# Performance work log

Hardware: AMD Instinct MI355X
Metric: run time of the kernel (lower is better)

## Reference

```python
import jax, jax.numpy as jnp
import numpy as np

B, C, H, W = 8, 256, 64, 64
CI = 128  # inter_channels = in_channels // reduction

def _conv1x1(x, w, b):
    # x: [b, c, h, w], w: [o, c], b: [o]
    return jnp.einsum('bchw,oc->bohw', x, w) + b[None, :, None, None]

def setup_inputs() -> dict:
    key = jax.random.key(0)
    ks = jax.random.split(key, 5)
    s_in = 1.0 / np.sqrt(C)
    s_ci = 1.0 / np.sqrt(CI)
    return {
        'x': jax.random.normal(ks[0], (B, C, H, W), jnp.float32),
        'w_g': jax.random.normal(ks[1], (CI, C), jnp.float32) * s_in,
        'b_g': jnp.zeros((CI,), jnp.float32),
        'w_theta': jax.random.normal(ks[2], (CI, C), jnp.float32) * s_in,
        'b_theta': jnp.zeros((CI,), jnp.float32),
        'w_phi': jax.random.normal(ks[3], (CI, C), jnp.float32) * s_in,
        'b_phi': jnp.zeros((CI,), jnp.float32),
        'w_out': jax.random.normal(ks[4], (C, CI), jnp.float32) * s_ci,
        'b_out': jnp.zeros((C,), jnp.float32),
    }

def reference(x, w_g, b_g, w_theta, b_theta, w_phi, b_phi, w_out, b_out):
    n, c, h, w = x.shape
    N = h * w
    g_x = _conv1x1(x, w_g, b_g).reshape(n, CI, N).transpose(0, 2, 1)        # [b, N, ci]
    theta_x = _conv1x1(x, w_theta, b_theta).reshape(n, CI, N).transpose(0, 2, 1)  # [b, N, ci]
    phi_x = _conv1x1(x, w_phi, b_phi).reshape(n, CI, N)                     # [b, ci, N]
    pw = jnp.einsum('bnc,bcm->bnm', theta_x, phi_x)                         # [b, N, N]
    # Faithful to source: divides by ci**(-0.5) == multiplies by sqrt(ci)
    pw = pw / (jnp.asarray(CI, x.dtype) ** -0.5)
    pw = jax.nn.softmax(pw, axis=-1)
    y = jnp.einsum('bnm,bmc->bnc', pw, g_x)                                 # [b, N, ci]
    y = y.transpose(0, 2, 1).reshape(n, CI, h, w)
    return x + _conv1x1(y, w_out, b_out)
```

## Files before the change

### kernel.cpp

```cpp
#include <hip/hip_runtime.h>
#include <hip/hip_bf16.h>
#include <stdint.h>
#include <stddef.h>


typedef __bf16 bf16;
typedef __attribute__((ext_vector_type(8))) __bf16 bf16x8;
typedef __attribute__((ext_vector_type(4))) __bf16 bf16x4;
typedef __attribute__((ext_vector_type(4))) float  f32x4;
typedef __attribute__((ext_vector_type(4))) int    i32x4;

#define MFMA16(a, b, c) __builtin_amdgcn_mfma_f32_16x16x32_bf16((a), (b), (c), 0, 0, 0)

constexpr int NB  = 8;
constexpr int NC  = 256;
constexpr int NN  = 4096;
constexpr int NCI = 128;
constexpr size_t NEL = (size_t)NB * NN * NCI;
constexpr int PBATCH = NN * NCI;

#define QSCALE (11.313708498984761f * 1.4426950408889634f)


__global__ __launch_bounds__(256) void k_proj(
    const float* __restrict__ x,
    const float* __restrict__ wt, const float* __restrict__ bt,
    const float* __restrict__ wp, const float* __restrict__ bp,
    const float* __restrict__ wg, const float* __restrict__ bg,
    bf16* __restrict__ qh, bf16* __restrict__ ql,
    bf16* __restrict__ kh, bf16* __restrict__ kl,
    bf16* __restrict__ vv)
{
    const int nt  = blockIdx.x;
    const int pj  = blockIdx.y;
    const int b   = blockIdx.z;
    const int tid = threadIdx.x;
    const int wv  = tid >> 6;
    const int ln  = tid & 63;
    const int lg  = ln >> 4;
    const int lq  = ln & 15;

    const float* W;
    const float* bias;
    if (pj == 0)      { W = wt; bias = bt; }
    else if (pj == 1) { W = wp; bias = bp; }
    else              { W = wg; bias = bg; }
    const bool split = (pj != 2);

    __shared__ char lds[49152];
    char* Ah = lds;
    char* Al = lds + 8192;
    char* Wh = lds + 16384;
    char* Wl = lds + 32768;

    f32x4 acc[8];
#pragma unroll
    for (int j = 0; j < 8; ++j) acc[j] = f32x4{0.f, 0.f, 0.f, 0.f};

    const int n0 = nt * 64;

    for (int c0 = 0; c0 < NC; c0 += 64) {
        __syncthreads();
#pragma unroll
        for (int p = 0; p < 4; ++p) {
            int cc = p * 16 + (tid >> 4);
            int nn = (tid & 15) * 4;
            f32x4 xv = *(const f32x4*)(x + ((size_t)b * NC + (c0 + cc)) * NN + n0 + nn);
#pragma unroll
            for (int e = 0; e < 4; ++e) {
                float f = xv[e];
                bf16 hh = (bf16)f;
                int row = nn + e;
                int off = (row * 128 + cc * 2) ^ ((row & 7) << 4);
                *(bf16*)(Ah + off) = hh;
                *(bf16*)(Al + off) = (bf16)(f - (float)hh);
            }
        }
#pragma unroll
        for (int p = 0; p < 8; ++p) {
            int i  = p * 16 + (tid >> 4);
            int c4 = (tid & 15) * 4;
            f32x4 w4 = *(const f32x4*)(W + (size_t)i * NC + c0 + c4);
            bf16x4 hv, lv;
#pragma unroll
            for (int e = 0; e < 4; ++e) {
                bf16 hh = (bf16)w4[e];
                hv[e] = hh;
                lv[e] = (bf16)(w4[e] - (float)hh);
            }
            int off = (i * 128 + c4 * 2) ^ ((i & 7) << 4);
            *(bf16x4*)(Wh + off) = hv;
            if (split) *(bf16x4*)(Wl + off) = lv;
        }
        __syncthreads();
#pragma unroll
        for (int kk = 0; kk < 2; ++kk) {
            int row  = wv * 16 + lq;
            int koff = kk * 64 + lg * 16;
            int aoff = (row * 128 + koff) ^ ((row & 7) << 4);
            bf16x8 ah = *(const bf16x8*)(Ah + aoff);
            bf16x8 al = *(const bf16x8*)(Al + aoff);
#pragma unroll
            for (int j = 0; j < 8; ++j) {
                int ir   = j * 16 + lq;
                int woff = (ir * 128 + koff) ^ ((ir & 7) << 4);
                bf16x8 bh = *(const bf16x8*)(Wh + woff);
                acc[j] = MFMA16(ah, bh, acc[j]);
                if (split) {
                    bf16x8 bl = *(const bf16x8*)(Wl + woff);
                    acc[j] = MFMA16(ah, bl, acc[j]);
                    acc[j] = MFMA16(al, bh, acc[j]);
                }
            }
        }
    }

    if (pj == 2) {
        __syncthreads();
        char* T = lds;
#pragma unroll
        for (int j = 0; j < 8; ++j) {
            int i = j * 16 + lq;
            float bv2 = bias[i];
#pragma unroll
            for (int r = 0; r < 4; ++r) {
                int nl = wv * 16 + lg * 4 + r;
                int off = (i * 128 + nl * 2) ^ ((i & 7) << 4);
                *(bf16*)(T + off) = (bf16)(acc[j][r] + bv2);
            }
        }
        __syncthreads();
#pragma unroll
        for (int p = 0; p < 4; ++p) {
            int i  = p * 32 + (tid >> 3);
            int sl = tid & 7;
            i32x4 tv = *(const i32x4*)(T + ((i * 128 + sl * 16) ^ ((i & 7) << 4)));
            size_t off = (size_t)b * PBATCH
                       + (size_t)((((nt * 8 + (i >> 4)) * 2 + (sl >> 2)) * 64
                                   + (sl & 3) * 16 + (i & 15)) * 8);
            *(i32x4*)(vv + off) = tv;
        }
    } else {
        const float sc = (pj == 0) ? QSCALE : 1.0f;
#pragma unroll
        for (int j = 0; j < 8; ++j) {
            int i = j * 16 + lq;
            float bv2 = bias[i];
#pragma unroll
            for (int r = 0; r < 4; ++r) {
                int q = n0 + wv * 16 + lg * 4 + r;
                size_t off = ((size_t)b * NN + q) * NCI + i;
                float val = (acc[j][r] + bv2) * sc;
                bf16 hh = (bf16)val;
                bf16 ll = (bf16)(val - (float)hh);
                if (pj == 0) { qh[off] = hh; ql[off] = ll; }
                else         { kh[off] = hh; kl[off] = ll; }
            }
        }
    }
}

__global__ __launch_bounds__(128, 2) void k_attn_sp(
    const bf16* __restrict__ qh, const bf16* __restrict__ ql,
    const bf16* __restrict__ kh, const bf16* __restrict__ kl,
    const bf16* __restrict__ vf,
    bf16* __restrict__ p0, bf16* __restrict__ p1, float* __restrict__ ml)
{
    const int bid = blockIdx.x;
    const int b   = bid & 7;
    const int rs  = bid >> 3;
    const int qt  = rs & 63;
    const int h   = rs >> 6;
    const int tid = threadIdx.x;
    const int wv  = tid >> 6;
    const int ln  = tid & 63;
    const int lg  = ln >> 4;
    const int lq  = ln & 15;
    const int n0  = qt * 64;
    const int mb0 = h * 2048;
    bf16* ph = h ? p1 : p0;

    __shared__ __attribute__((aligned(16))) char lds[36864];
    char* P = lds + 32768 + wv * 2048;

    const int smm = tid >> 4;
    const int ssl = tid & 15;

    bf16x8 qhf[2][4], qlf[2][4];
#pragma unroll
    for (int q2 = 0; q2 < 2; ++q2) {
        int qrow = n0 + wv * 32 + q2 * 16 + lq;
        const bf16* bh = qh + ((size_t)b * NN + qrow) * NCI;
        const bf16* bl = ql + ((size_t)b * NN + qrow) * NCI;
#pragma unroll
        for (int kk = 0; kk < 4; ++kk) {
            qhf[q2][kk] = *(const bf16x8*)(bh + kk * 32 + lg * 8);
            qlf[q2][kk] = *(const bf16x8*)(bl + kk * 32 + lg * 8);
        }
    }

    f32x4 o[2][8];
#pragma unroll
    for (int q2 = 0; q2 < 2; ++q2)
#pragma unroll
        for (int j = 0; j < 8; ++j) o[q2][j] = f32x4{0.f, 0.f, 0.f, 0.f};
    float mrun[2] = {-1e30f, -1e30f};
    float lrun[2] = {0.f, 0.f};

    const bf16* vb = vf + (size_t)b * PBATCH + (size_t)ln * 8;

    {
#pragma unroll
        for (int p = 0; p < 4; ++p) {
            int mm = p * 8 + smm;
            size_t g = ((size_t)b * NN + mb0 + mm) * NCI + ssl * 8;
            i32x4 hv = *(const i32x4*)(kh + g);
            i32x4 lv = *(const i32x4*)(kl + g);
            int off = (mm * 256 + ssl * 16) ^ ((mm & 7) << 4);
            *(i32x4*)(lds + off) = hv;
            *(i32x4*)(lds + 8192 + off) = lv;
        }
    }
    __syncthreads();

    for (int t = 0; t < 64; ++t) {
        const int cur = t & 1;
        char* KHc = lds + cur * 16384;
        char* KLc = KHc + 8192;
        char* KHn = lds + (cur ^ 1) * 16384;
        char* KLn = KHn + 8192;
        const bool pre = (t < 63);

        i32x4 rkh[4], rkl[4];
        if (pre) {
#pragma unroll
            for (int p = 0; p < 4; ++p) {
                size_t g = ((size_t)b * NN + mb0 + (t + 1) * 32 + p * 8 + smm) * NCI + ssl * 8;
                rkh[p] = *(const i32x4*)(kh + g);
                rkl[p] = *(const i32x4*)(kl + g);
            }
        }
        __builtin_amdgcn_sched_barrier(0);

        f32x4 s[2][2];
        __builtin_amdgcn_s_setprio(1);
#pragma unroll
        for (int jm = 0; jm < 2; ++jm) {
            s[jm][0] = f32x4{0.f, 0.f, 0.f, 0.f};
            s[jm][1] = f32x4{0.f, 0.f, 0.f, 0.f};
            const int mrow = jm * 16 + lq;
            const int sw = (mrow & 7) << 4;
#pragma unroll
            for (int kk = 0; kk < 4; ++kk) {
                int aoff = (mrow * 256 + kk * 64 + lg * 16) ^ sw;
                bf16x8 ah = *(const bf16x8*)(KHc + aoff);
                bf16x8 al = *(const bf16x8*)(KLc + aoff);
                s[jm][0] = MFMA16(ah, qhf[0][kk], s[jm][0]);
                s[jm][1] = MFMA16(ah, qhf[1][kk], s[jm][1]);
                s[jm][0] = MFMA16(al, qhf[0][kk], s[jm][0]);
                s[jm][1] = MFMA16(al, qhf[1][kk], s[jm][1]);
                s[jm][0] = MFMA16(ah, qlf[0][kk], s[jm][0]);
                s[jm][1] = MFMA16(ah, qlf[1][kk], s[jm][1]);
            }
        }
        __builtin_amdgcn_s_setprio(0);

        bf16x8 bv[8];
        {
            const bf16* vp = vb + (size_t)(h * 32 + (t >> 1)) * 8192;
#pragma unroll
            for (int j = 0; j < 8; ++j)
                bv[j] = *(const bf16x8*)(vp + (j * 2 + (t & 1)) * 512);
        }
        __builtin_amdgcn_sched_barrier(0);

        if (pre) {
#pragma unroll
            for (int p = 0; p < 4; ++p) {
                int mm = p * 8 + smm;
                int off = (mm * 256 + ssl * 16) ^ ((mm & 7) << 4);
                *(i32x4*)(KHn + off) = rkh[p];
                *(i32x4*)(KLn + off) = rkl[p];
            }
        }

        float tm[2];
        tm[0] = s[0][0][0];
        tm[1] = s[0][1][0];
#pragma unroll
        for (int jm = 0; jm < 2; ++jm)
#pragma unroll
            for (int r = 0; r < 4; ++r) {
                tm[0] = fmaxf(tm[0], s[jm][0][r]);
                tm[1] = fmaxf(tm[1], s[jm][1][r]);
            }
#pragma unroll
        for (int q2 = 0; q2 < 2; ++q2) {
            tm[q2] = fmaxf(tm[q2], __shfl_xor(tm[q2], 16));
            tm[q2] = fmaxf(tm[q2], __shfl_xor(tm[q2], 32));
        }

        bool grow = (tm[0] > mrun[0] + 8.f) || (tm[1] > mrun[1] + 8.f);
        if (__any(grow)) {
            float alpha[2];
#pragma unroll
            for (int q2 = 0; q2 < 2; ++q2) {
                float mnew = fmaxf(mrun[q2], tm[q2]);
                alpha[q2] = exp2f(mrun[q2] - mnew);
                mrun[q2] = mnew;
                lrun[q2] *= alpha[q2];
            }
            float av0[4], av1[4];
#pragma unroll
            for (int r = 0; r < 4; ++r) {
                av0[r] = __shfl(alpha[0], lg * 4 + r);
                av1[r] = __shfl(alpha[1], lg * 4 + r);
            }
#pragma unroll
            for (int j = 0; j < 8; ++j)
#pragma unroll
                for (int r = 0; r < 4; ++r) {
                    o[0][j][r] *= av0[r];
                    o[1][j][r] *= av1[r];
                }
        }

        float psum[2] = {0.f, 0.f};
#pragma unroll
        for (int jm = 0; jm < 2; ++jm)
#pragma unroll
            for (int q2 = 0; q2 < 2; ++q2) {
                bf16x4 pk;
#pragma unroll
                for (int r = 0; r < 4; ++r) {
                    float e2 = exp2f(s[jm][q2][r] - mrun[q2]);
                    psum[q2] += e2;
                    pk[r] = (bf16)e2;
                }
                int row = q2 * 16 + lq;
                int off = (row * 64 + (jm * 16 + lg * 4) * 2) ^ ((row & 7) << 4);
                *(bf16x4*)(P + off) = pk;
            }
#pragma unroll
        for (int q2 = 0; q2 < 2; ++q2) {
            psum[q2] += __shfl_xor(psum[q2], 16);
            psum[q2] += __shfl_xor(psum[q2], 32);
            lrun[q2] += psum[q2];
        }

        bf16x8 pa[2];
#pragma unroll
        for (int q2 = 0; q2 < 2; ++q2) {
            int row = q2 * 16 + lq;
            pa[q2] = *(const bf16x8*)(P + ((row * 64 + lg * 16) ^ ((row & 7) << 4)));
        }
        __builtin_amdgcn_s_setprio(1);
#pragma unroll
        for (int j = 0; j < 8; ++j) {
            o[0][j] = MFMA16(pa[0], bv[j], o[0][j]);
            o[1][j] = MFMA16(pa[1], bv[j], o[1][j]);
        }
        __builtin_amdgcn_s_setprio(0);

        __syncthreads();
    }

    float rl0[4], rl1[4];
#pragma unroll
    for (int r = 0; r < 4; ++r) {
        rl0[r] = 1.f / __shfl(lrun[0], lg * 4 + r);
        rl1[r] = 1.f / __shfl(lrun[1], lg * 4 + r);
    }
#pragma unroll
    for (int j = 0; j < 8; ++j) {
        int d = j * 16 + lq;
#pragma unroll
        for (int r = 0; r < 4; ++r) {
            int q0 = n0 + wv * 32 + lg * 4 + r;
            ph[((size_t)b * NN + q0) * NCI + d]      = (bf16)(o[0][j][r] * rl0[r]);
            ph[((size_t)b * NN + q0 + 16) * NCI + d] = (bf16)(o[1][j][r] * rl1[r]);
        }
    }
    if (lg == 0) {
#pragma unroll
        for (int q2 = 0; q2 < 2; ++q2) {
            int row = n0 + wv * 32 + q2 * 16 + lq;
            size_t base = ((size_t)b * NN + row) * 4 + h * 2;
            ml[base]     = mrun[q2];
            ml[base + 1] = lrun[q2];
        }
    }
}

__global__ __launch_bounds__(256) void k_comb(
    const bf16* __restrict__ p0, const bf16* __restrict__ p1,
    const float* __restrict__ ml, bf16* __restrict__ y)
{
    int row = blockIdx.x * 16 + (threadIdx.x >> 4);
    int d0  = (threadIdx.x & 15) * 8;
    f32x4 q = *(const f32x4*)(ml + (size_t)row * 4);
    float M  = fmaxf(q[0], q[2]);
    float w0 = exp2f(q[0] - M) * q[1];
    float w1 = exp2f(q[2] - M) * q[3];
    float inv = 1.f / (w0 + w1);
    w0 *= inv; w1 *= inv;
    size_t off = (size_t)row * NCI + d0;
    bf16x8 a = *(const bf16x8*)(p0 + off);
    bf16x8 c = *(const bf16x8*)(p1 + off);
    bf16x8 r;
#pragma unroll
    for (int e = 0; e < 8; ++e) r[e] = (bf16)(w0 * (float)a[e] + w1 * (float)c[e]);
    *(bf16x8*)(y + off) = r;
}

__global__ __launch_bounds__(256) void k_out(
    const bf16* __restrict__ y, const float* __restrict__ x,
    const float* __restrict__ w_out, const float* __restrict__ b_out,
    float* __restrict__ out)
{
    const int nt  = blockIdx.x;
    const int b   = blockIdx.y;
    const int tid = threadIdx.x;
    const int wv  = tid >> 6;
    const int ln  = tid & 63;
    const int lg  = ln >> 4;
    const int lq  = ln & 15;
    const int n0  = nt * 64;

    __shared__ char Y[16384];
#pragma unroll
    for (int p = 0; p < 4; ++p) {
        int nn = p * 16 + (tid >> 4);
        int d0 = (tid & 15) * 8;
        i32x4 t = *(const i32x4*)(y + ((size_t)b * NN + n0 + nn) * NCI + d0);
        *(i32x4*)(Y + ((nn * 256 + d0 * 2) ^ ((nn & 7) << 4))) = t;
    }
    __syncthreads();

    bf16x8 af[4];
    {
        int row = wv * 16 + lq;
#pragma unroll
        for (int kk = 0; kk < 4; ++kk) {
            int koff = kk * 64 + lg * 16;
            af[kk] = *(const bf16x8*)(Y + ((row * 256 + koff) ^ ((row & 7) << 4)));
        }
    }

    f32x4 acc[16];
#pragma unroll
    for (int j = 0; j < 16; ++j) acc[j] = f32x4{0.f, 0.f, 0.f, 0.f};

#pragma unroll
    for (int j = 0; j < 16; ++j) {
        int c = j * 16 + lq;
#pragma unroll
        for (int kk = 0; kk < 4; ++kk) {
            int i0 = kk * 32 + lg * 8;
            f32x4 wa = *(const f32x4*)(w_out + (size_t)c * NCI + i0);
            f32x4 wb = *(const f32x4*)(w_out + (size_t)c * NCI + i0 + 4);
            bf16x8 bw;
#pragma unroll
            for (int e = 0; e < 4; ++e) { bw[e] = (bf16)wa[e]; bw[e + 4] = (bf16)wb[e]; }
            acc[j] = MFMA16(af[kk], bw, acc[j]);
        }
    }

#pragma unroll
    for (int j = 0; j < 16; ++j) {
        int c = j * 16 + lq;
        int nb = n0 + wv * 16 + lg * 4;
        size_t off = ((size_t)b * NC + c) * (size_t)NN + nb;
        f32x4 xv = *(const f32x4*)(x + off);
        float bo = b_out[c];
        f32x4 r;
#pragma unroll
        for (int t = 0; t < 4; ++t) r[t] = acc[j][t] + xv[t] + bo;
        *(f32x4*)(out + off) = r;
    }
}

extern "C" void kernel_launch(void* const* d_in, const int* in_sizes, int n_in,
                              void* d_out, int out_size, void* d_ws, size_t ws_size,
                              hipStream_t stream)
{
    (void)in_sizes; (void)n_in; (void)out_size; (void)ws_size;
    const float* x  = (const float*)d_in[0];
    const float* wg = (const float*)d_in[1];
    const float* bg = (const float*)d_in[2];
    const float* wt = (const float*)d_in[3];
    const float* bt = (const float*)d_in[4];
    const float* wp = (const float*)d_in[5];
    const float* bp = (const float*)d_in[6];
    const float* wo = (const float*)d_in[7];
    const float* bo = (const float*)d_in[8];
    float* out = (float*)d_out;

    char* ws = (char*)d_ws;
    bf16* qh = (bf16*)(ws);
    bf16* ql = (bf16*)(ws + NEL * 2);
    bf16* kh = (bf16*)(ws + NEL * 4);
    bf16* kl = (bf16*)(ws + NEL * 6);
    bf16* vv = (bf16*)(ws + NEL * 8);
    bf16* y  = qh;
    bf16* p0 = (bf16*)(ws + NEL * 10);
    bf16* p1 = (bf16*)(ws + NEL * 12);
    float* ml = (float*)(ws + NEL * 14);

    k_proj<<<dim3(64, 3, 8), 256, 0, stream>>>(x, wt, bt, wp, bp, wg, bg,
                                               qh, ql, kh, kl, vv);
    k_attn_sp<<<dim3(1024), 128, 0, stream>>>(qh, ql, kh, kl, vv, p0, p1, ml);
    k_comb<<<dim3(2048), 256, 0, stream>>>(p0, p1, ml, y);
    k_out<<<dim3(64, 8), 256, 0, stream>>>(y, x, wo, bo, out);
}
```

Baseline: 249.5 us.

## Fuse three projections per block, fold split-combine into output conv, hoist V loads

```diff
diff --git a/kernel.cpp b/kernel.cpp
--- a/kernel.cpp
+++ b/kernel.cpp
@@ -22,7 +22,7 @@
 #define QSCALE (11.313708498984761f * 1.4426950408889634f)
 
 
-__global__ __launch_bounds__(256) void k_proj(
+__global__ __launch_bounds__(256) void k_proj3(
     const float* __restrict__ x,
     const float* __restrict__ wt, const float* __restrict__ bt,
     const float* __restrict__ wp, const float* __restrict__ bp,
@@ -32,30 +32,24 @@
     bf16* __restrict__ vv)
 {
     const int nt  = blockIdx.x;
-    const int pj  = blockIdx.y;
-    const int b   = blockIdx.z;
+    const int b   = blockIdx.y;
     const int tid = threadIdx.x;
     const int wv  = tid >> 6;
     const int ln  = tid & 63;
     const int lg  = ln >> 4;
     const int lq  = ln & 15;
 
-    const float* W;
-    const float* bias;
-    if (pj == 0)      { W = wt; bias = bt; }
-    else if (pj == 1) { W = wp; bias = bp; }
-    else              { W = wg; bias = bg; }
-    const bool split = (pj != 2);
-
     __shared__ char lds[49152];
     char* Ah = lds;
     char* Al = lds + 8192;
     char* Wh = lds + 16384;
     char* Wl = lds + 32768;
 
-    f32x4 acc[8];
-#pragma unroll
-    for (int j = 0; j < 8; ++j) acc[j] = f32x4{0.f, 0.f, 0.f, 0.f};
+    f32x4 acc[3][8];
+#pragma unroll
+    for (int pj = 0; pj < 3; ++pj)
+#pragma unroll
+        for (int j = 0; j < 8; ++j) acc[pj][j] = f32x4{0.f, 0.f, 0.f, 0.f};
 
     const int n0 = nt * 64;
 
@@ -76,87 +70,93 @@
                 *(bf16*)(Al + off) = (bf16)(f - (float)hh);
             }
         }
-#pragma unroll
-        for (int p = 0; p < 8; ++p) {
-            int i  = p * 16 + (tid >> 4);
-            int c4 = (tid & 15) * 4;
-            f32x4 w4 = *(const f32x4*)(W + (size_t)i * NC + c0 + c4);
-            bf16x4 hv, lv;
-#pragma unroll
-            for (int e = 0; e < 4; ++e) {
-                bf16 hh = (bf16)w4[e];
-                hv[e] = hh;
-                lv[e] = (bf16)(w4[e] - (float)hh);
-            }
-            int off = (i * 128 + c4 * 2) ^ ((i & 7) << 4);
-            *(bf16x4*)(Wh + off) = hv;
-            if (split) *(bf16x4*)(Wl + off) = lv;
-        }
-        __syncthreads();
-#pragma unroll
-        for (int kk = 0; kk < 2; ++kk) {
-            int row  = wv * 16 + lq;
-            int koff = kk * 64 + lg * 16;
-            int aoff = (row * 128 + koff) ^ ((row & 7) << 4);
-            bf16x8 ah = *(const bf16x8*)(Ah + aoff);
-            bf16x8 al = *(const bf16x8*)(Al + aoff);
-#pragma unroll
-            for (int j = 0; j < 8; ++j) {
-                int ir   = j * 16 + lq;
-                int woff = (ir * 128 + koff) ^ ((ir & 7) << 4);
-                bf16x8 bh = *(const bf16x8*)(Wh + woff);
-                acc[j] = MFMA16(ah, bh, acc[j]);
-                if (split) {
-                    bf16x8 bl = *(const bf16x8*)(Wl + woff);
-                    acc[j] = MFMA16(ah, bl, acc[j]);
-                    acc[j] = MFMA16(al, bh, acc[j]);
+
+#pragma unroll
+        for (int pj = 0; pj < 3; ++pj) {
+            const float* W = (pj == 0) ? wt : (pj == 1) ? wp : wg;
+            const bool split = (pj != 2);
+            if (pj != 0) __syncthreads();
+#pragma unroll
+            for (int p = 0; p < 8; ++p) {
+                int i  = p * 16 + (tid >> 4);
+                int c4 = (tid & 15) * 4;
+                f32x4 w4 = *(const f32x4*)(W + (size_t)i * NC + c0 + c4);
+                bf16x4 hv, lv;
+#pragma unroll
+                for (int e = 0; e < 4; ++e) {
+                    bf16 hh = (bf16)w4[e];
+                    hv[e] = hh;
+                    lv[e] = (bf16)(w4[e] - (float)hh);
                 }
-            }
-        }
-    }
-
-    if (pj == 2) {
-        __syncthreads();
-        char* T = lds;
-#pragma unroll
-        for (int j = 0; j < 8; ++j) {
-            int i = j * 16 + lq;
-            float bv2 = bias[i];
-#pragma unroll
-            for (int r = 0; r < 4; ++r) {
-                int nl = wv * 16 + lg * 4 + r;
-                int off = (i * 128 + nl * 2) ^ ((i & 7) << 4);
-                *(bf16*)(T + off) = (bf16)(acc[j][r] + bv2);
-            }
-        }
-        __syncthreads();
-#pragma unroll
-        for (int p = 0; p < 4; ++p) {
-            int i  = p * 32 + (tid >> 3);
-            int sl = tid & 7;
-            i32x4 tv = *(const i32x4*)(T + ((i * 128 + sl * 16) ^ ((i & 7) << 4)));
-            size_t off = (size_t)b * PBATCH
-                       + (size_t)((((nt * 8 + (i >> 4)) * 2 + (sl >> 2)) * 64
-                                   + (sl & 3) * 16 + (i & 15)) * 8);
-            *(i32x4*)(vv + off) = tv;
-        }
-    } else {
-        const float sc = (pj == 0) ? QSCALE : 1.0f;
-#pragma unroll
-        for (int j = 0; j < 8; ++j) {
-            int i = j * 16 + lq;
-            float bv2 = bias[i];
-#pragma unroll
-            for (int r = 0; r < 4; ++r) {
-                int q = n0 + wv * 16 + lg * 4 + r;
-                size_t off = ((size_t)b * NN + q) * NCI + i;
-                float val = (acc[j][r] + bv2) * sc;
-                bf16 hh = (bf16)val;
-                bf16 ll = (bf16)(val - (float)hh);
-                if (pj == 0) { qh[off] = hh; ql[off] = ll; }
-                else         { kh[off] = hh; kl[off] = ll; }
-            }
-        }
+                int off = (i * 128 + c4 * 2) ^ ((i & 7) << 4);
+                *(bf16x4*)(Wh + off) = hv;
+                if (split) *(bf16x4*)(Wl + off) = lv;
+            }
+            __syncthreads();
+#pragma unroll
+            for (int kk = 0; kk < 2; ++kk) {
+                int row  = wv * 16 + lq;
+                int koff = kk * 64 + lg * 16;
+                int aoff = (row * 128 + koff) ^ ((row & 7) << 4);
+                bf16x8 ah = *(const bf16x8*)(Ah + aoff);
+                bf16x8 al = *(const bf16x8*)(Al + aoff);
+#pragma unroll
+                for (int j = 0; j < 8; ++j) {
+                    int ir   = j * 16 + lq;
+                    int woff = (ir * 128 + koff) ^ ((ir & 7) << 4);
+                    bf16x8 bh = *(const bf16x8*)(Wh + woff);
+                    acc[pj][j] = MFMA16(ah, bh, acc[pj][j]);
+                    if (split) {
+                        bf16x8 bl = *(const bf16x8*)(Wl + woff);
+                        acc[pj][j] = MFMA16(ah, bl, acc[pj][j]);
+                        acc[pj][j] = MFMA16(al, bh, acc[pj][j]);
+                    }
+                }
+            }
+        }
+    }
+
+#pragma unroll
+    for (int j = 0; j < 8; ++j) {
+        int i = j * 16 + lq;
+        float bvt = bt[i];
+        float bvp = bp[i];
+#pragma unroll
+        for (int r = 0; r < 4; ++r) {
+            int q = n0 + wv * 16 + lg * 4 + r;
+            size_t off = ((size_t)b * NN + q) * NCI + i;
+            float vt2 = (acc[0][j][r] + bvt) * QSCALE;
+            bf16 th = (bf16)vt2;
+            qh[off] = th; ql[off] = (bf16)(vt2 - (float)th);
+            float vp2 = acc[1][j][r] + bvp;
+            bf16 phh = (bf16)vp2;
+            kh[off] = phh; kl[off] = (bf16)(vp2 - (float)phh);
+        }
+    }
+
+    __syncthreads();
+    char* T = lds;
+#pragma unroll
+    for (int j = 0; j < 8; ++j) {
+        int i = j * 16 + lq;
+        float bv2 = bg[i];
+#pragma unroll
+        for (int r = 0; r < 4; ++r) {
+            int nl = wv * 16 + lg * 4 + r;
+            int off = (i * 128 + nl * 2) ^ ((i & 7) << 4);
+            *(bf16*)(T + off) = (bf16)(acc[2][j][r] + bv2);
+        }
+    }
+    __syncthreads();
+#pragma unroll
+    for (int p = 0; p < 4; ++p) {
+        int i  = p * 32 + (tid >> 3);
+        int sl = tid & 7;
+        i32x4 tv = *(const i32x4*)(T + ((i * 128 + sl * 16) ^ ((i & 7) << 4)));
+        size_t off = (size_t)b * PBATCH
+                   + (size_t)((((nt * 8 + (i >> 4)) * 2 + (sl >> 2)) * 64
+                               + (sl & 3) * 16 + (i & 15)) * 8);
+        *(i32x4*)(vv + off) = tv;
     }
 }
 
@@ -240,6 +240,13 @@
                 rkl[p] = *(const i32x4*)(kl + g);
             }
         }
+        bf16x8 bv[8];
+        {
+            const bf16* vp = vb + (size_t)(h * 32 + (t >> 1)) * 8192;
+#pragma unroll
+            for (int j = 0; j < 8; ++j)
+                bv[j] = *(const bf16x8*)(vp + (j * 2 + (t & 1)) * 512);
+        }
         __builtin_amdgcn_sched_barrier(0);
 
         f32x4 s[2][2];
@@ -265,15 +272,6 @@
         }
         __builtin_amdgcn_s_setprio(0);
 
-        bf16x8 bv[8];
-        {
-            const bf16* vp = vb + (size_t)(h * 32 + (t >> 1)) * 8192;
-#pragma unroll
-            for (int j = 0; j < 8; ++j)
-                bv[j] = *(const bf16x8*)(vp + (j * 2 + (t & 1)) * 512);
-        }
-        __builtin_amdgcn_sched_barrier(0);
-
         if (pre) {
 #pragma unroll
             for (int p = 0; p < 4; ++p) {
@@ -392,29 +390,9 @@
     }
 }
 
-__global__ __launch_bounds__(256) void k_comb(
+__global__ __launch_bounds__(256) void k_out(
     const bf16* __restrict__ p0, const bf16* __restrict__ p1,
-    const float* __restrict__ ml, bf16* __restrict__ y)
-{
-    int row = blockIdx.x * 16 + (threadIdx.x >> 4);
-    int d0  = (threadIdx.x & 15) * 8;
-    f32x4 q = *(const f32x4*)(ml + (size_t)row * 4);
-    float M  = fmaxf(q[0], q[2]);
-    float w0 = exp2f(q[0] - M) * q[1];
-    float w1 = exp2f(q[2] - M) * q[3];
-    float inv = 1.f / (w0 + w1);
-    w0 *= inv; w1 *= inv;
-    size_t off = (size_t)row * NCI + d0;
-    bf16x8 a = *(const bf16x8*)(p0 + off);
-    bf16x8 c = *(const bf16x8*)(p1 + off);
-    bf16x8 r;
-#pragma unroll
-    for (int e = 0; e < 8; ++e) r[e] = (bf16)(w0 * (float)a[e] + w1 * (float)c[e]);
-    *(bf16x8*)(y + off) = r;
-}
-
-__global__ __launch_bounds__(256) void k_out(
-    const bf16* __restrict__ y, const float* __restrict__ x,
+    const float* __restrict__ ml, const float* __restrict__ x,
     const float* __restrict__ w_out, const float* __restrict__ b_out,
     float* __restrict__ out)
 {
@@ -432,8 +410,21 @@
     for (int p = 0; p < 4; ++p) {
         int nn = p * 16 + (tid >> 4);
         int d0 = (tid & 15) * 8;
-        i32x4 t = *(const i32x4*)(y + ((size_t)b * NN + n0 + nn) * NCI + d0);
-        *(i32x4*)(Y + ((nn * 256 + d0 * 2) ^ ((nn & 7) << 4))) = t;
+        size_t row = (size_t)b * NN + n0 + nn;
+        f32x4 q = *(const f32x4*)(ml + row * 4);
+        float M  = fmaxf(q[0], q[2]);
+        float w0 = exp2f(q[0] - M) * q[1];
+        float w1 = exp2f(q[2] - M) * q[3];
+        float inv = 1.f / (w0 + w1);
+        w0 *= inv; w1 *= inv;
+        size_t off = row * NCI + d0;
+        bf16x8 a = *(const bf16x8*)(p0 + off);
+        bf16x8 c = *(const bf16x8*)(p1 + off);
+        bf16x8 rr;
+#pragma unroll
+        for (int e = 0; e < 8; ++e)
+            rr[e] = (bf16)(w0 * (float)a[e] + w1 * (float)c[e]);
+        *(bf16x8*)(Y + ((nn * 256 + d0 * 2) ^ ((nn & 7) << 4))) = rr;
     }
     __syncthreads();
 
@@ -502,14 +493,12 @@
     bf16* kh = (bf16*)(ws + NEL * 4);
     bf16* kl = (bf16*)(ws + NEL * 6);
     bf16* vv = (bf16*)(ws + NEL * 8);
-    bf16* y  = qh;
     bf16* p0 = (bf16*)(ws + NEL * 10);
     bf16* p1 = (bf16*)(ws + NEL * 12);
     float* ml = (float*)(ws + NEL * 14);
 
-    k_proj<<<dim3(64, 3, 8), 256, 0, stream>>>(x, wt, bt, wp, bp, wg, bg,
-                                               qh, ql, kh, kl, vv);
+    k_proj3<<<dim3(64, 8), 256, 0, stream>>>(x, wt, bt, wp, bp, wg, bg,
+                                             qh, ql, kh, kl, vv);
     k_attn_sp<<<dim3(1024), 128, 0, stream>>>(qh, ql, kh, kl, vv, p0, p1, ml);
-    k_comb<<<dim3(2048), 256, 0, stream>>>(p0, p1, ml, y);
-    k_out<<<dim3(64, 8), 256, 0, stream>>>(y, x, wo, bo, out);
+    k_out<<<dim3(64, 8), 256, 0, stream>>>(p0, p1, ml, x, wo, bo, out);
 }
```

Result: no change. 253.7 us (+1.7%).
